# Kernel optimization log

Hardware: AMD Instinct MI355X
Metric: run time of the kernel (lower is better)

## Reference

```python
import jax, jax.numpy as jnp
import numpy as np

EPS = 1e-5
NUM_HEADS = 8

def _inorm(x):
    # InstanceNorm1d (affine=False): normalize over last (length) axis per (B, C)
    m = x.mean(axis=-1, keepdims=True)
    v = x.var(axis=-1, keepdims=True)  # biased variance, as torch instance norm
    return (x - m) * jax.lax.rsqrt(v + EPS)

def setup_inputs() -> dict:
    key = jax.random.key(0)
    ks = jax.random.split(key, 12)
    B, Nl, HW = 4, 1024, 4096
    Cl, Cv, Ck, Cval, Cout = 512, 512, 256, 256, 256
    w = lambda k, shape: (jax.random.normal(k, shape, jnp.float32) * 0.02)
    return {
        "l": jax.random.normal(ks[0], (B, Nl, Cl), jnp.float32),
        "x": jax.random.normal(ks[1], (B, HW, Cv), jnp.float32),
        "Wq": w(ks[2], (Ck, Cl)),   "bq": w(ks[3], (Ck,)),
        "Wk": w(ks[4], (Ck, Cv)),   "bk": w(ks[5], (Ck,)),
        "Wv": w(ks[6], (Cval, Cv)), "bv": w(ks[7], (Cval,)),
        "Ww": w(ks[8], (Cout, Cval)), "bw": w(ks[9], (Cout,)),
    }

def reference(l, x, Wq, bq, Wk, bk, Wv, bv, Ww, bw):
    H = NUM_HEADS
    Ck = Wq.shape[0]
    Cv = Wv.shape[0]
    dk, dv = Ck // H, Cv // H
    B, Nl, _ = l.shape
    HW = x.shape[1]

    # 1x1 Conv1d == per-position linear
    q = jnp.einsum('blc,kc->blk', l, Wq) + bq                     # [B, Nl, Ck]
    k = jnp.einsum('bnc,kc->bkn', x, Wk) + bk[None, :, None]      # [B, Ck, HW]
    k = _inorm(k)                                                  # InstanceNorm over HW
    v = jnp.einsum('bnc,kc->bkn', x, Wv) + bv[None, :, None]      # [B, Cv, HW]

    q = q.reshape(B, Nl, H, dk).transpose(0, 2, 1, 3)             # [B, H, Nl, dk]
    k = k.reshape(B, H, dk, HW)                                   # [B, H, dk, HW]
    v = v.reshape(B, H, dv, HW)                                   # [B, H, dv, HW]

    sim = jnp.einsum('bhld,bhdn->bhln', q, k) * (Ck ** -0.5)      # [B, H, Nl, HW]
    att = jax.nn.softmax(sim, axis=-1)
    out = jnp.einsum('bhln,bhdn->bhld', att, v)                   # [B, H, Nl, dv]

    out = out.transpose(0, 2, 1, 3).reshape(B, Nl, Cv)            # [B, Nl, Cv]
    out = jnp.einsum('blc,oc->bol', out, Ww) + bw[None, :, None]  # [B, Cout, Nl]
    out = _inorm(out)                                              # InstanceNorm over Nl
    return out.transpose(0, 2, 1)                                  # [B, Nl, Cout]
```

## Files before the change

### kernel.cpp

```cpp
#include <hip/hip_runtime.h>

constexpr int Bn = 4, NL = 1024, HWn = 4096, NH = 8;

typedef __attribute__((ext_vector_type(8))) short bf16x8;
typedef __attribute__((ext_vector_type(4))) float f32x4;
#define MFMA16 __builtin_amdgcn_mfma_f32_16x16x32_bf16

extern "C" __device__ float __ocml_native_exp2_f32(float);

__device__ __forceinline__ float b2f(unsigned short u) {
  union { unsigned int i; float f; } x; x.i = ((unsigned int)u) << 16; return x.f;
}
__device__ __forceinline__ unsigned short f2b(float f) {
  union { float f; unsigned int i; } x; x.f = f;
  unsigned int r = x.i + 0x7fffu + ((x.i >> 16) & 1u);
  return (unsigned short)(r >> 16);
}

__device__ __forceinline__ void async_load16(const unsigned short* g, unsigned short* l) {
  __builtin_amdgcn_global_load_lds(
      (const __attribute__((address_space(1))) unsigned int*)g,
      (__attribute__((address_space(3))) unsigned int*)l, 16, 0, 0);
}

__global__ __launch_bounds__(256) void convall(const float* __restrict__ x,
    const float* __restrict__ l,
    const float* __restrict__ Wk, const float* __restrict__ Wv,
    const float* __restrict__ Wq, const float* __restrict__ Ww,
    unsigned short* __restrict__ xbf, unsigned short* __restrict__ lbf,
    unsigned short* __restrict__ wkb, unsigned short* __restrict__ wvb,
    unsigned short* __restrict__ wqb,
    unsigned short* __restrict__ wwh, unsigned short* __restrict__ wwl,
    float* __restrict__ Fz)
{
  const int id = blockIdx.x, tid = threadIdx.x;
  if (id < 8192) {
    int i = (id * 256 + tid) * 4;
    float4 v = *(const float4*)(x + i);
    ushort4 o; o.x = f2b(v.x); o.y = f2b(v.y); o.z = f2b(v.z); o.w = f2b(v.w);
    *(ushort4*)(xbf + i) = o;
  } else if (id < 10240) {
    int i = ((id - 8192) * 256 + tid) * 4;
    float4 v = *(const float4*)(l + i);
    ushort4 o; o.x = f2b(v.x); o.y = f2b(v.y); o.z = f2b(v.z); o.w = f2b(v.w);
    *(ushort4*)(lbf + i) = o;
  } else if (id < 10752) {
    int sub = id - 10240;
    int y = sub >> 7, bx = sub & 127;
    int i = (bx * 256 + tid) * 4;
    if (y == 3) {
      if (i >= 65536) return;
      float4 v = *(const float4*)(Ww + i);
      ushort4 hi, lo;
      hi.x = f2b(v.x); lo.x = f2b(v.x - b2f(hi.x));
      hi.y = f2b(v.y); lo.y = f2b(v.y - b2f(hi.y));
      hi.z = f2b(v.z); lo.z = f2b(v.z - b2f(hi.z));
      hi.w = f2b(v.w); lo.w = f2b(v.w - b2f(hi.w));
      *(ushort4*)(wwh + i) = hi;
      *(ushort4*)(wwl + i) = lo;
      return;
    }
    const float* src = y == 0 ? Wk : (y == 1 ? Wv : Wq);
    unsigned short* dst = y == 0 ? wkb : (y == 1 ? wvb : wqb);
    float4 v = *(const float4*)(src + i);
    ushort4 o; o.x = f2b(v.x); o.y = f2b(v.y); o.z = f2b(v.z); o.w = f2b(v.w);
    *(ushort4*)(dst + i) = o;
  } else {
    int i = (id - 10752) * 1024 + tid * 4;
    *(float4*)(Fz + i) = (float4){0.f, 0.f, 0.f, 0.f};
  }
}

__global__ __launch_bounds__(256, 3) void gemm128(
    const unsigned short* __restrict__ xbf, const unsigned short* __restrict__ lbf,
    const unsigned short* __restrict__ wkb, const unsigned short* __restrict__ wvb,
    const unsigned short* __restrict__ wqb,
    const float* __restrict__ bk, const float* __restrict__ bv, const float* __restrict__ bq,
    unsigned short* __restrict__ khb, unsigned short* __restrict__ vfrag,
    unsigned short* __restrict__ qbuf,
    float* __restrict__ ksum, float* __restrict__ kss, float* __restrict__ vcs)
{
  __shared__ unsigned short sh[16384];
  unsigned short* As0 = sh;
  unsigned short* Bs0 = sh + 8192;
  const int id = blockIdx.x;
  const int mode = id < 256 ? 0 : (id < 512 ? 1 : 2);
  const int local = id - (mode == 0 ? 0 : (mode == 1 ? 256 : 512));
  const int rb = local >> 1, cb = local & 1;
  const int m0 = rb * 128, n0 = cb * 128;
  const unsigned short* A = (mode == 2) ? lbf : xbf;
  const unsigned short* W = (mode == 0) ? wkb : (mode == 1 ? wvb : wqb);
  const float* bias = (mode == 0) ? bk : (mode == 1 ? bv : bq);

  const int tid = threadIdx.x, w = tid >> 6, lane = tid & 63;
  const int quad = lane >> 4, l15 = lane & 15;
  const int wr = w >> 1, wc = w & 1;

  const int p0 = tid, p1 = tid + 256;
  const int am0 = p0 >> 2, ak0 = (p0 & 3) * 8;
  const int am1 = p1 >> 2, ak1 = (p1 & 3) * 8;

  f32x4 acc[4][4];
#pragma unroll
  for (int i = 0; i < 4; ++i)
#pragma unroll
    for (int j = 0; j < 4; ++j) acc[i][j] = (f32x4){0.f, 0.f, 0.f, 0.f};

  async_load16(A + (size_t)(m0 + am0) * 512 + ak0, &As0[p0 * 8]);
  async_load16(A + (size_t)(m0 + am1) * 512 + ak1, &As0[p1 * 8]);
  async_load16(W + (size_t)(n0 + am0) * 512 + ak0, &Bs0[p0 * 8]);
  async_load16(W + (size_t)(n0 + am1) * 512 + ak1, &Bs0[p1 * 8]);

  for (int kt = 0; kt < 16; ++kt) {
    const int cur = kt & 1;
    __syncthreads();
    if (kt < 15) {
      int k0 = (kt + 1) * 32;
      int nx = (cur ^ 1) * 4096;
      async_load16(A + (size_t)(m0 + am0) * 512 + k0 + ak0, &As0[nx + p0 * 8]);
      async_load16(A + (size_t)(m0 + am1) * 512 + k0 + ak1, &As0[nx + p1 * 8]);
      async_load16(W + (size_t)(n0 + am0) * 512 + k0 + ak0, &Bs0[nx + p0 * 8]);
      async_load16(W + (size_t)(n0 + am1) * 512 + k0 + ak1, &Bs0[nx + p1 * 8]);
    }
    bf16x8 af[4], bf[4];
#pragma unroll
    for (int fr = 0; fr < 4; ++fr)
      af[fr] = *(const bf16x8*)&As0[cur * 4096 + (wr * 64 + fr * 16 + l15) * 32 + quad * 8];
#pragma unroll
    for (int fc = 0; fc < 4; ++fc)
      bf[fc] = *(const bf16x8*)&Bs0[cur * 4096 + (wc * 64 + fc * 16 + l15) * 32 + quad * 8];
#pragma unroll
    for (int fr = 0; fr < 4; ++fr)
#pragma unroll
      for (int fc = 0; fc < 4; ++fc)
        acc[fr][fc] = MFMA16(af[fr], bf[fc], acc[fr][fc], 0, 0, 0);
  }

  float bb[4];
#pragma unroll
  for (int fc = 0; fc < 4; ++fc) bb[fc] = bias[n0 + wc * 64 + fc * 16 + l15];

  if (mode != 2) {
    const int b = m0 >> 12;
    const int seg = (m0 & 4095) >> 9;
#pragma unroll
    for (int fc = 0; fc < 4; ++fc) {
      float s = 0.f, ssq = 0.f;
#pragma unroll
      for (int fr = 0; fr < 4; ++fr)
#pragma unroll
        for (int r = 0; r < 4; ++r) {
          float v = acc[fr][fc][r] + bb[fc];
          s += v; ssq += v * v;
        }
      s += __shfl_xor(s, 16); s += __shfl_xor(s, 32);
      if (mode == 0) {
        ssq += __shfl_xor(ssq, 16); ssq += __shfl_xor(ssq, 32);
        if (quad == 0) {
          int col = n0 + wc * 64 + fc * 16 + l15;
          atomicAdd(&ksum[b * 256 + col], s);
          atomicAdd(&kss[b * 256 + col], ssq);
        }
      } else if (quad == 0) {
        int col = n0 + wc * 64 + fc * 16 + l15;
        atomicAdd(&vcs[seg * 1024 + b * 256 + col], s);
      }
    }
  }

  if (mode == 1) {
    __syncthreads();
#pragma unroll
    for (int fc = 0; fc < 4; ++fc) {
      const int ls = wr * 4 + wc * 2 + ((fc * 16 + l15) >> 5);
      const int dvt = fc & 1;
#pragma unroll
      for (int fr = 0; fr < 4; ++fr) {
#pragma unroll
        for (int r = 0; r < 4; ++r) {
          int kappa = 4 * (quad * 4 + r) + fr;
          int kh2 = kappa >> 5, lq = (kappa >> 3) & 3, j = kappa & 7;
          sh[ls * 2048 + kh2 * 1024 + dvt * 512 + lq * 128 + l15 * 8 + j] =
              f2b(acc[fr][fc][r] + bb[fc]);
        }
      }
    }
    __syncthreads();
    const int b2 = m0 >> 12, h0 = cb * 4, seg64b = (m0 & 4095) >> 6;
#pragma unroll
    for (int i = 0; i < 8; ++i) {
      int p = i * 256 + tid;
      int ls = p >> 8, off8 = (p & 255) * 8;
      int dh = ls & 3, wr2 = ls >> 2;
      size_t dst = ((size_t)((b2 * 8 + h0 + dh) * 64) + seg64b + wr2) * 2048 + off8;
      *(bf16x8*)(vfrag + dst) = *(const bf16x8*)&sh[ls * 2048 + off8];
    }
  } else {
    unsigned short* dst = (mode == 0) ? khb : qbuf;
#pragma unroll
    for (int fr = 0; fr < 4; ++fr) {
#pragma unroll
      for (int fc = 0; fc < 4; ++fc) {
        int col = n0 + wc * 64 + fc * 16 + l15;
#pragma unroll
        for (int r = 0; r < 4; ++r) {
          int row = m0 + wr * 64 + fr * 16 + quad * 4 + r;
          unsigned short val = f2b(acc[fr][fc][r] + bb[fc]);
          if (mode == 2) {
            dst[(size_t)row * 256 + col] = val;
          } else {
            int b = row >> 12, n = row & 4095, h = col >> 5, d = col & 31;
            dst[((size_t)(b * 8 + h) * 4096 + n) * 32 + d] = val;
          }
        }
      }
    }
  }
}

__global__ __launch_bounds__(256, 2) void attn11(const unsigned short* __restrict__ qbuf,
    const unsigned short* __restrict__ khb, const unsigned short* __restrict__ vfrag,
    const float* __restrict__ ksum, const float* __restrict__ kss,
    const float* __restrict__ vcs,
    unsigned short* __restrict__ aoh, unsigned short* __restrict__ aol)
{
  const int bh = blockIdx.x, b = bh >> 3, h = bh & 7;
  const int lsuper = blockIdx.y;
  const int tid = threadIdx.x, w = tid >> 6, lane = tid & 63;
  const int quad = lane >> 4, l15 = lane & 15;

  __shared__ unsigned short ps[4][16][64];

  bf16x8 qa;
  {
    float fold[8];
    const int ch = bh * 32 + quad * 8;
#pragma unroll
    for (int j = 0; j < 8; ++j) {
      float m = ksum[ch + j] * (1.f / 4096.f);
      float var = kss[ch + j] * (1.f / 4096.f) - m * m;
      fold[j] = rsqrtf(var + 1e-5f) * (0.0625f * 1.44269504f);
    }
    int l = lsuper * 64 + w * 16 + l15;
    bf16x8 qr = *(const bf16x8*)(qbuf + ((size_t)(b * NL + l)) * 256 + h * 32 + quad * 8);
    const unsigned short* qq = (const unsigned short*)&qr;
    unsigned short tmp[8];
#pragma unroll
    for (int j = 0; j < 8; ++j) tmp[j] = f2b(b2f(qq[j]) * fold[j]);
    qa = *(const bf16x8*)tmp;
  }

  float drow[4] = {0.f, 0.f, 0.f, 0.f};
  f32x4 acc[2];
  acc[0] = (f32x4){0.f,0.f,0.f,0.f};
  acc[1] = (f32x4){0.f,0.f,0.f,0.f};

  const unsigned short* kl = khb + (size_t)bh * 131072 + l15 * 32 + quad * 8;
  const unsigned short* vl = vfrag + (size_t)bh * 131072 + lane * 8;

  unsigned short* psw = &ps[w][0][0];
  const unsigned rdswz = (unsigned)((l15 & 7) << 4);

  for (int c = 0; c < 64; ++c) {
    bf16x8 kb[4], vb[4];
#pragma unroll
    for (int t = 0; t < 4; ++t)
      kb[t] = *(const bf16x8*)(kl + c * 2048 + t * 512);
#pragma unroll
    for (int i = 0; i < 4; ++i)
      vb[i] = *(const bf16x8*)(vl + c * 2048 + i * 512);

    const f32x4 z = (f32x4){0.f,0.f,0.f,0.f};
    f32x4 sv[4];
    __builtin_amdgcn_s_setprio(1);
#pragma unroll
    for (int t = 0; t < 4; ++t) sv[t] = MFMA16(qa, kb[t], z, 0, 0, 0);
    __builtin_amdgcn_s_setprio(0);
#pragma unroll
    for (int r = 0; r < 4; ++r) {
      float x0 = __ocml_native_exp2_f32(sv[0][r]);
      float x1 = __ocml_native_exp2_f32(sv[1][r]);
      float x2 = __ocml_native_exp2_f32(sv[2][r]);
      float x3 = __ocml_native_exp2_f32(sv[3][r]);
      drow[r] += (x0 + x1) + (x2 + x3);
      unsigned pk0, pk1;
      asm("v_cvt_pk_bf16_f32 %0, %1, %2" : "=v"(pk0) : "v"(x0 - 1.0f), "v"(x1 - 1.0f));
      asm("v_cvt_pk_bf16_f32 %0, %1, %2" : "=v"(pk1) : "v"(x2 - 1.0f), "v"(x3 - 1.0f));
      const int row = quad * 4 + r;
      unsigned off = (unsigned)((l15 * 8) ^ ((row & 7) << 4));
      uint2 pk; pk.x = pk0; pk.y = pk1;
      *(uint2*)((char*)(psw + row * 64) + off) = pk;
    }
    asm volatile("s_waitcnt lgkmcnt(0)" ::: "memory");
    __builtin_amdgcn_s_setprio(1);
#pragma unroll
    for (int kh2 = 0; kh2 < 2; ++kh2) {
      unsigned off = (unsigned)((kh2 * 64 + quad * 16) ^ rdswz);
      bf16x8 pa = *(const bf16x8*)((const char*)(psw + l15 * 64) + off);
      acc[0] = MFMA16(pa, vb[kh2 * 2 + 0], acc[0], 0, 0, 0);
      acc[1] = MFMA16(pa, vb[kh2 * 2 + 1], acc[1], 0, 0, 0);
    }
    __builtin_amdgcn_s_setprio(0);
  }

  float cs0 = 0.f, cs1 = 0.f;
#pragma unroll
  for (int s = 0; s < 8; ++s) {
    cs0 += vcs[s * 1024 + bh * 32 + l15];
    cs1 += vcs[s * 1024 + bh * 32 + 16 + l15];
  }

#pragma unroll
  for (int r = 0; r < 4; ++r) {
    float sv = drow[r];
    sv += __shfl_xor(sv, 1, 16);
    sv += __shfl_xor(sv, 2, 16);
    sv += __shfl_xor(sv, 4, 16);
    sv += __shfl_xor(sv, 8, 16);
    int l = lsuper * 64 + w * 16 + quad * 4 + r;
    size_t idx = ((size_t)(b * NL) + l) * 256 + h * 32;
    float o0 = (acc[0][r] + cs0) / sv;
    float o1 = (acc[1][r] + cs1) / sv;
    unsigned short h0s = f2b(o0);
    unsigned short h1s = f2b(o1);
    aoh[idx + l15]      = h0s;
    aol[idx + l15]      = f2b(o0 - b2f(h0s));
    aoh[idx + 16 + l15] = h1s;
    aol[idx + 16 + l15] = f2b(o1 - b2f(h1s));
  }
}

__global__ __launch_bounds__(256) void gemm_proj(
    const unsigned short* __restrict__ aoh, const unsigned short* __restrict__ aol,
    const unsigned short* __restrict__ wwh, const unsigned short* __restrict__ wwl,
    const float* __restrict__ bw, float* __restrict__ pj,
    float* __restrict__ psum, float* __restrict__ psq)
{
  __shared__ unsigned short As[2][2048];
  __shared__ unsigned short Bs[2][2048];
  const int bm = blockIdx.x * 64, bn = blockIdx.y * 64;
  const int tid = threadIdx.x, w = tid >> 6, lane = tid & 63;
  const int quad = lane >> 4, l15 = lane & 15;
  const int wr = w >> 1, wc = w & 1;
  const int arow = tid >> 2, apiece = (tid & 3) * 8;

  f32x4 acc[2][2];
#pragma unroll
  for (int i = 0; i < 2; ++i)
#pragma unroll
    for (int j = 0; j < 2; ++j) acc[i][j] = (f32x4){0.f, 0.f, 0.f, 0.f};

  async_load16(aoh + (size_t)(bm + arow) * 256 + apiece, &As[0][tid * 8]);
  async_load16(wwh + (size_t)(bn + arow) * 256 + apiece, &Bs[0][tid * 8]);

  for (int it = 0; it < 24; ++it) {
    const int cur = it & 1;
    __syncthreads();
    if (it < 23) {
      int nx = it + 1;
      int p = nx >> 3;
      const unsigned short* An = (p == 1) ? aol : aoh;
      const unsigned short* Bm = (p == 2) ? wwl : wwh;
      int k0 = (nx & 7) * 32;
      async_load16(An + (size_t)(bm + arow) * 256 + k0 + apiece, &As[cur ^ 1][tid * 8]);
      async_load16(Bm + (size_t)(bn + arow) * 256 + k0 + apiece, &Bs[cur ^ 1][tid * 8]);
    }
    bf16x8 af[2], bf[2];
#pragma unroll
    for (int fr = 0; fr < 2; ++fr)
      af[fr] = *(const bf16x8*)&As[cur][(wr * 32 + fr * 16 + l15) * 32 + quad * 8];
#pragma unroll
    for (int fc = 0; fc < 2; ++fc)
      bf[fc] = *(const bf16x8*)&Bs[cur][(wc * 32 + fc * 16 + l15) * 32 + quad * 8];
#pragma unroll
    for (int fr = 0; fr < 2; ++fr)
#pragma unroll
      for (int fc = 0; fc < 2; ++fc)
        acc[fr][fc] = MFMA16(af[fr], bf[fc], acc[fr][fc], 0, 0, 0);
  }

  const int b = bm >> 10;
#pragma unroll
  for (int fr = 0; fr < 2; ++fr)
#pragma unroll
    for (int fc = 0; fc < 2; ++fc) {
      int col = bn + wc * 32 + fc * 16 + l15;
      float bb = bw[col];
      float s = 0.f, ssq = 0.f;
#pragma unroll
      for (int r = 0; r < 4; ++r) {
        int row = bm + wr * 32 + fr * 16 + quad * 4 + r;
        float v = acc[fr][fc][r] + bb;
        pj[(size_t)row * 256 + col] = v;
        s += v; ssq += v * v;
      }
      s += __shfl_xor(s, 16); s += __shfl_xor(s, 32);
      ssq += __shfl_xor(ssq, 16); ssq += __shfl_xor(ssq, 32);
      if (quad == 0) {
        atomicAdd(&psum[b * 256 + col], s);
        atomicAdd(&psq[b * 256 + col], ssq);
      }
    }
}

__global__ __launch_bounds__(256) void final_out(const float* __restrict__ proj,
    const float* __restrict__ psum, const float* __restrict__ psq,
    float* __restrict__ out)
{
  const int b = blockIdx.x, o = threadIdx.x;
  const int l1 = blockIdx.y * 16;
  const float m = psum[b * 256 + o] * (1.f / 1024.f);
  const float r = rsqrtf(psq[b * 256 + o] * (1.f / 1024.f) - m * m + 1e-5f);
  for (int i = 0; i < 16; ++i) {
    size_t idx = ((size_t)(b * NL + l1 + i)) * 256 + o;
    out[idx] = (proj[idx] - m) * r;
  }
}

extern "C" void kernel_launch(void* const* d_in, const int* in_sizes, int n_in,
                              void* d_out, int out_size, void* d_ws, size_t ws_size,
                              hipStream_t stream)
{
  const float* l  = (const float*)d_in[0];
  const float* x  = (const float*)d_in[1];
  const float* Wq = (const float*)d_in[2];
  const float* bq = (const float*)d_in[3];
  const float* Wk = (const float*)d_in[4];
  const float* bk = (const float*)d_in[5];
  const float* Wv = (const float*)d_in[6];
  const float* bv = (const float*)d_in[7];
  const float* Ww = (const float*)d_in[8];
  const float* bw = (const float*)d_in[9];
  float* out = (float*)d_out;

  unsigned short* up = (unsigned short*)d_ws;
  unsigned short* xbf   = up;
  unsigned short* lbf   = xbf   + 8388608;
  unsigned short* wkb   = lbf   + 2097152;
  unsigned short* wvb   = wkb   + 131072;
  unsigned short* wqb   = wvb   + 131072;
  unsigned short* qbuf  = wqb   + 131072;
  unsigned short* khb   = qbuf  + 1048576;
  unsigned short* vhb   = khb   + 4194304;
  unsigned short* vfrag = vhb   + 4194304;
  unsigned short* aoh   = vfrag + 4194304;
  unsigned short* aol   = aoh   + 1048576;
  unsigned short* wwh   = aol   + 1048576;
  unsigned short* wwl   = wwh   + 65536;
  float* F     = (float*)((char*)d_ws + 53477376);
  float* ksum  = F;
  float* kss   = F + 1024;
  float* vcs   = F + 2048;
  float* psum  = F + 10240;
  float* psq   = F + 11264;
  float* pj    = F + 15360;

  dim3 blk(256);
  convall<<<10764, blk, 0, stream>>>(x, l, Wk, Wv, Wq, Ww, xbf, lbf,
                                     wkb, wvb, wqb, wwh, wwl, F);
  gemm128<<<576, blk, 0, stream>>>(xbf, lbf, wkb, wvb, wqb, bk, bv, bq,
                                   khb, vfrag, qbuf, ksum, kss, vcs);
  attn11<<<dim3(32, 16), blk, 0, stream>>>(qbuf, khb, vfrag, ksum, kss, vcs, aoh, aol);
  gemm_proj<<<dim3(64, 4), blk, 0, stream>>>(aoh, aol, wwh, wwl, bw, pj, psum, psq);
  final_out<<<dim3(4, 64), blk, 0, stream>>>(pj, psum, psq, out);
}
```

Measured before the change: 177.0 us.

## Split attention key sequence across two wave groups and combine partials in LDS

The attention kernel now uses 512 threads per block. Two halves of 4 waves each process half of the HW key range (32 chunks each) for the same 64 query rows. The second half writes its partial output accumulators and softmax denominators to shared memory, and after a barrier the first half combines them and writes the final normalized output. This doubles the number of active waves and halves the serial loop length, to fix low occupancy with only 512 blocks. The cost is extra LDS, a block-wide sync and a combine step.

```diff
diff --git a/kernel.cpp b/kernel.cpp
--- a/kernel.cpp
+++ b/kernel.cpp
@@ -218,7 +218,7 @@
   }
 }
 
-__global__ __launch_bounds__(256, 2) void attn11(const unsigned short* __restrict__ qbuf,
+__global__ __launch_bounds__(512, 4) void attn12(const unsigned short* __restrict__ qbuf,
     const unsigned short* __restrict__ khb, const unsigned short* __restrict__ vfrag,
     const float* __restrict__ ksum, const float* __restrict__ kss,
     const float* __restrict__ vcs,
@@ -227,9 +227,12 @@
   const int bh = blockIdx.x, b = bh >> 3, h = bh & 7;
   const int lsuper = blockIdx.y;
   const int tid = threadIdx.x, w = tid >> 6, lane = tid & 63;
+  const int half = w >> 2, wsub = w & 3;
   const int quad = lane >> 4, l15 = lane & 15;
 
-  __shared__ unsigned short ps[4][16][64];
+  __shared__ unsigned short ps[8][16][64];
+  __shared__ float comb[4][16][32];
+  __shared__ float combD[4][16];
 
   bf16x8 qa;
   {
@@ -241,7 +244,7 @@
       float var = kss[ch + j] * (1.f / 4096.f) - m * m;
       fold[j] = rsqrtf(var + 1e-5f) * (0.0625f * 1.44269504f);
     }
-    int l = lsuper * 64 + w * 16 + l15;
+    int l = lsuper * 64 + wsub * 16 + l15;
     bf16x8 qr = *(const bf16x8*)(qbuf + ((size_t)(b * NL + l)) * 256 + h * 32 + quad * 8);
     const unsigned short* qq = (const unsigned short*)&qr;
     unsigned short tmp[8];
@@ -255,13 +258,16 @@
   acc[0] = (f32x4){0.f,0.f,0.f,0.f};
   acc[1] = (f32x4){0.f,0.f,0.f,0.f};
 
-  const unsigned short* kl = khb + (size_t)bh * 131072 + l15 * 32 + quad * 8;
-  const unsigned short* vl = vfrag + (size_t)bh * 131072 + lane * 8;
+  const int c0 = half * 32;
+  const unsigned short* kl = khb + (size_t)bh * 131072 + (size_t)c0 * 2048
+                             + l15 * 32 + quad * 8;
+  const unsigned short* vl = vfrag + (size_t)bh * 131072 + (size_t)c0 * 2048
+                             + lane * 8;
 
   unsigned short* psw = &ps[w][0][0];
   const unsigned rdswz = (unsigned)((l15 & 7) << 4);
 
-  for (int c = 0; c < 64; ++c) {
+  for (int c = 0; c < 32; ++c) {
     bf16x8 kb[4], vb[4];
 #pragma unroll
     for (int t = 0; t < 4; ++t)
@@ -305,11 +311,13 @@
 
   float cs0 = 0.f, cs1 = 0.f;
 #pragma unroll
-  for (int s = 0; s < 8; ++s) {
-    cs0 += vcs[s * 1024 + bh * 32 + l15];
-    cs1 += vcs[s * 1024 + bh * 32 + 16 + l15];
-  }
-
+  for (int s = 0; s < 4; ++s) {
+    int seg = half * 4 + s;
+    cs0 += vcs[seg * 1024 + bh * 32 + l15];
+    cs1 += vcs[seg * 1024 + bh * 32 + 16 + l15];
+  }
+
+  float svv[4];
 #pragma unroll
   for (int r = 0; r < 4; ++r) {
     float sv = drow[r];
@@ -317,16 +325,37 @@
     sv += __shfl_xor(sv, 2, 16);
     sv += __shfl_xor(sv, 4, 16);
     sv += __shfl_xor(sv, 8, 16);
-    int l = lsuper * 64 + w * 16 + quad * 4 + r;
-    size_t idx = ((size_t)(b * NL) + l) * 256 + h * 32;
-    float o0 = (acc[0][r] + cs0) / sv;
-    float o1 = (acc[1][r] + cs1) / sv;
-    unsigned short h0s = f2b(o0);
-    unsigned short h1s = f2b(o1);
-    aoh[idx + l15]      = h0s;
-    aol[idx + l15]      = f2b(o0 - b2f(h0s));
-    aoh[idx + 16 + l15] = h1s;
-    aol[idx + 16 + l15] = f2b(o1 - b2f(h1s));
+    svv[r] = sv;
+    acc[0][r] += cs0;
+    acc[1][r] += cs1;
+  }
+
+  if (half == 1) {
+#pragma unroll
+    for (int r = 0; r < 4; ++r) {
+      int row16 = quad * 4 + r;
+      comb[wsub][row16][l15]      = acc[0][r];
+      comb[wsub][row16][16 + l15] = acc[1][r];
+      if (l15 == 0) combD[wsub][row16] = svv[r];
+    }
+  }
+  __syncthreads();
+  if (half == 0) {
+#pragma unroll
+    for (int r = 0; r < 4; ++r) {
+      int row16 = quad * 4 + r;
+      float d  = svv[r] + combD[wsub][row16];
+      float o0 = (acc[0][r] + comb[wsub][row16][l15]) / d;
+      float o1 = (acc[1][r] + comb[wsub][row16][16 + l15]) / d;
+      int l = lsuper * 64 + wsub * 16 + row16;
+      size_t idx = ((size_t)(b * NL) + l) * 256 + h * 32;
+      unsigned short h0s = f2b(o0);
+      unsigned short h1s = f2b(o1);
+      aoh[idx + l15]      = h0s;
+      aol[idx + l15]      = f2b(o0 - b2f(h0s));
+      aoh[idx + 16 + l15] = h1s;
+      aol[idx + 16 + l15] = f2b(o1 - b2f(h1s));
+    }
   }
 }
 
@@ -460,7 +489,8 @@
                                      wkb, wvb, wqb, wwh, wwl, F);
   gemm128<<<576, blk, 0, stream>>>(xbf, lbf, wkb, wvb, wqb, bk, bv, bq,
                                    khb, vfrag, qbuf, ksum, kss, vcs);
-  attn11<<<dim3(32, 16), blk, 0, stream>>>(qbuf, khb, vfrag, ksum, kss, vcs, aoh, aol);
+  attn12<<<dim3(32, 16), dim3(512), 0, stream>>>(qbuf, khb, vfrag, ksum, kss, vcs,
+                                                 aoh, aol);
   gemm_proj<<<dim3(64, 4), blk, 0, stream>>>(aoh, aol, wwh, wwl, bw, pj, psum, psq);
   final_out<<<dim3(4, 64), blk, 0, stream>>>(pj, psum, psq, out);
 }
```

New measurement: 182.7 us. 3.2% more time.
